# Kernel optimization log

Hardware: AMD Instinct MI355X
Metric: run time of the kernel (lower is better)

## Reference

```python
import jax, jax.numpy as jnp
import numpy as np

DIM = 2048
DIM_HEAD = 128
HEADS = 16
FF_INNER = 4 * DIM  # 8192
ATTN_INNER = DIM_HEAD * HEADS  # 2048
FUSED_DIMS = (ATTN_INNER, DIM_HEAD, DIM_HEAD, FF_INNER * 2)
R = 8
B, N = 2, 2048


def setup_inputs() -> dict:
    key = jax.random.key(0)
    ks = jax.random.split(key, 12)
    s = 0.02
    return {
        "x": jax.random.normal(ks[0], (B, N, DIM), jnp.float32),
        "gamma": jnp.ones((DIM,), jnp.float32),
        "w_fused": jax.random.normal(ks[1], (DIM, sum(FUSED_DIMS)), jnp.float32) * s,
        "w_attn_out": jax.random.normal(ks[2], (ATTN_INNER, DIM), jnp.float32) * s,
        "w_ff_out": jax.random.normal(ks[3], (FF_INNER, DIM), jnp.float32) * s,
        "a_q": jax.random.normal(ks[4], (DIM, R), jnp.float32) * s,
        "b_q": jax.random.normal(ks[5], (R, ATTN_INNER), jnp.float32) * s,
        "a_k": jax.random.normal(ks[6], (DIM, R), jnp.float32) * s,
        "b_k": jax.random.normal(ks[7], (R, DIM_HEAD), jnp.float32) * s,
        "a_v": jax.random.normal(ks[8], (DIM, R), jnp.float32) * s,
        "b_v": jax.random.normal(ks[9], (R, DIM_HEAD), jnp.float32) * s,
        "a_o": jax.random.normal(ks[10], (ATTN_INNER, R), jnp.float32) * s,
        "b_o": jax.random.normal(ks[11], (R, DIM), jnp.float32) * s,
    }


def _rotate_half(t):
    t1, t2 = jnp.split(t, 2, axis=-1)
    return jnp.concatenate((-t2, t1), axis=-1)


def _rope(pos, t):
    return t * jnp.cos(pos) + _rotate_half(t) * jnp.sin(pos)


def reference(x, gamma, w_fused, w_attn_out, w_ff_out,
              a_q, b_q, a_k, b_k, a_v, b_v, a_o, b_o):
    b, n, d = x.shape
    # LayerNorm (beta buffer is zeros)
    mu = jnp.mean(x, -1, keepdims=True)
    var = jnp.var(x, -1, keepdims=True)
    xn = (x - mu) * jax.lax.rsqrt(var + 1e-5) * gamma

    proj = xn @ w_fused
    splits = np.cumsum(FUSED_DIMS)[:-1]
    q, k, v, ff = jnp.split(proj, splits, axis=-1)

    # fused QKV LoRA (scale alpha/r = 1)
    q = q + (xn @ a_q) @ b_q
    k = k + (xn @ a_k) @ b_k
    v = v + (xn @ a_v) @ b_v

    q = q.reshape(b, n, HEADS, DIM_HEAD).transpose(0, 2, 1, 3)  # b h n d
    q = q * (DIM_HEAD ** -0.5)

    # rotary embedding
    inv_freq = 1.0 / (10000.0 ** (jnp.arange(0, DIM_HEAD, 2, dtype=jnp.float32) / DIM_HEAD))
    freqs = jnp.arange(n, dtype=jnp.float32)[:, None] * inv_freq[None, :]  # n, d/2
    pos = jnp.concatenate((freqs, freqs), axis=-1)  # n, d
    q = _rope(pos, q)          # broadcast over b,h
    k = _rope(pos, k)          # b n d (single head, MQA)

    sim = jnp.einsum('bhid,bjd->bhij', q, k)
    causal = jnp.triu(jnp.ones((n, n), dtype=bool), 1)
    sim = jnp.where(causal, -jnp.finfo(sim.dtype).max, sim)
    attn = jax.nn.softmax(sim, axis=-1)
    out = jnp.einsum('bhij,bjd->bhid', attn, v)
    out = out.transpose(0, 2, 1, 3).reshape(b, n, ATTN_INNER)

    attn_out = out @ w_attn_out + (out @ a_o) @ b_o

    x1, gate = jnp.split(ff, 2, axis=-1)
    ff_out = (jax.nn.silu(gate) * x1) @ w_ff_out
    return attn_out + ff_out
```

## Files before the change

kernel.cpp:

```cpp
#include <hip/hip_runtime.h>

typedef unsigned short u16;
typedef __attribute__((ext_vector_type(8))) short s8v;
typedef __attribute__((ext_vector_type(4))) float f32x4;

__device__ __forceinline__ u16 f2bf(float f) {
  unsigned int u = __float_as_uint(f);
  u += ((u >> 16) & 1u) + 0x7FFFu;
  return (u16)(u >> 16);
}
__device__ __forceinline__ float bf2f(u16 h) {
  return __uint_as_float(((unsigned int)h) << 16);
}
__device__ __forceinline__ void gl_lds16(const void* g, void* l) {
  __builtin_amdgcn_global_load_lds(
      (__attribute__((address_space(1))) void*)g,
      (__attribute__((address_space(3))) void*)l, 16, 0, 0);
}
__device__ __forceinline__ f32x4 mfma16(s8v a, s8v b, f32x4 c) {
  return __builtin_amdgcn_mfma_f32_16x16x32_bf16(a, b, c, 0, 0, 0);
}

__global__ void transpose_cvt(const float* __restrict__ in, u16* __restrict__ out,
                              int rows, int cols, int ldo) {
  __shared__ float tile[32][33];
  int c0 = blockIdx.x * 32, r0 = blockIdx.y * 32;
  int tx = threadIdx.x, ty = threadIdx.y;
#pragma unroll
  for (int i = 0; i < 4; i++)
    tile[ty + i * 8][tx] = in[(long)(r0 + ty + i * 8) * cols + c0 + tx];
  __syncthreads();
#pragma unroll
  for (int i = 0; i < 4; i++)
    out[(long)(c0 + ty + i * 8) * ldo + r0 + tx] = f2bf(tile[tx][ty + i * 8]);
}

__global__ void vtrans(const u16* __restrict__ proj, u16* __restrict__ v_t) {
  __shared__ u16 tile[32][33];
  int n0 = blockIdx.x * 32, d0 = blockIdx.y * 32, b = blockIdx.z;
  int tx = threadIdx.x, ty = threadIdx.y;
#pragma unroll
  for (int i = 0; i < 4; i++)
    tile[ty + i * 8][tx] =
        proj[((long)b * 2048 + n0 + ty + i * 8) * 18688 + 2176 + d0 + tx];
  __syncthreads();
#pragma unroll
  for (int i = 0; i < 4; i++)
    v_t[((long)b * 128 + d0 + ty + i * 8) * 2048 + n0 + tx] = tile[tx][ty + i * 8];
}

__global__ void fill_aug_k(u16* __restrict__ wt, int N, int ldo, int naug,
                           const float* __restrict__ bq, const float* __restrict__ bk,
                           const float* __restrict__ bv) {
  long idx = (long)blockIdx.x * 256 + threadIdx.x;
  if (idx >= (long)N * naug) return;
  int n = (int)(idx / naug), j = (int)(idx % naug);
  float v = 0.f;
  if (bq && j < 8 && n < 2048) v = bq[j * 2048 + n];
  else if (bk && j >= 8 && j < 16 && n >= 2048 && n < 2176) v = bk[(j - 8) * 128 + (n - 2048)];
  else if (bv && j >= 16 && j < 24 && n >= 2176 && n < 2304) v = bv[(j - 16) * 128 + (n - 2176)];
  wt[(long)n * ldo + 2048 + j] = f2bf(v);
}

__global__ __launch_bounds__(256) void layernorm_k(const float* __restrict__ x,
                                                   const float* __restrict__ gamma,
                                                   u16* __restrict__ xn) {
  const int row = blockIdx.x, tid = threadIdx.x;
  const float* xr = x + (long)row * 2048 + tid * 8;
  float4 v0 = *(const float4*)xr;
  float4 v1 = *(const float4*)(xr + 4);
  float vals[8] = {v0.x, v0.y, v0.z, v0.w, v1.x, v1.y, v1.z, v1.w};
  float s = 0.f, q = 0.f;
#pragma unroll
  for (int e = 0; e < 8; e++) { s += vals[e]; q += vals[e] * vals[e]; }
#pragma unroll
  for (int off = 32; off > 0; off >>= 1) {
    s += __shfl_down(s, off, 64);
    q += __shfl_down(q, off, 64);
  }
  __shared__ float red[8];
  const int w = tid >> 6, lane = tid & 63;
  if (lane == 0) { red[w] = s; red[4 + w] = q; }
  __syncthreads();
  if (tid == 0) {
    float S = red[0] + red[1] + red[2] + red[3];
    float Q = red[4] + red[5] + red[6] + red[7];
    float mu = S * (1.f / 2048.f);
    float var = Q * (1.f / 2048.f) - mu * mu;
    red[0] = mu; red[1] = rsqrtf(var + 1e-5f);
  }
  __syncthreads();
  float mu = red[0], rs = red[1];
  const float* g = gamma + tid * 8;
  u16 ov[8];
#pragma unroll
  for (int e = 0; e < 8; e++) ov[e] = f2bf((vals[e] - mu) * rs * g[e]);
  *(s8v*)(xn + (long)row * 2112 + tid * 8) = *(const s8v*)ov;
}

__global__ __launch_bounds__(256) void lora_down_x(u16* __restrict__ xn_aug,
                                                   const float* __restrict__ aq,
                                                   const float* __restrict__ ak,
                                                   const float* __restrict__ av) {
  const int row = blockIdx.x, tid = threadIdx.x;
  s8v xv = *(const s8v*)(xn_aug + (long)row * 2112 + tid * 8);
  float acc[3][8];
#pragma unroll
  for (int m = 0; m < 3; m++)
#pragma unroll
    for (int j = 0; j < 8; j++) acc[m][j] = 0.f;
  const float* mats[3] = {aq, ak, av};
#pragma unroll
  for (int e = 0; e < 8; e++) {
    float xe = bf2f((u16)xv[e]);
    int k = tid * 8 + e;
#pragma unroll
    for (int m = 0; m < 3; m++) {
      const float4* ap = (const float4*)(mats[m] + (long)k * 8);
      float4 a0 = ap[0], a1 = ap[1];
      acc[m][0] += xe * a0.x; acc[m][1] += xe * a0.y;
      acc[m][2] += xe * a0.z; acc[m][3] += xe * a0.w;
      acc[m][4] += xe * a1.x; acc[m][5] += xe * a1.y;
      acc[m][6] += xe * a1.z; acc[m][7] += xe * a1.w;
    }
  }
#pragma unroll
  for (int m = 0; m < 3; m++)
#pragma unroll
    for (int j = 0; j < 8; j++)
#pragma unroll
      for (int off = 32; off > 0; off >>= 1)
        acc[m][j] += __shfl_down(acc[m][j], off, 64);
  __shared__ float red[4][24];
  const int w = tid >> 6, lane = tid & 63;
  if (lane == 0)
    for (int m = 0; m < 3; m++)
      for (int j = 0; j < 8; j++) red[w][m * 8 + j] = acc[m][j];
  __syncthreads();
  if (tid < 64) {
    float v = 0.f;
    if (tid < 24) v = red[0][tid] + red[1][tid] + red[2][tid] + red[3][tid];
    xn_aug[(long)row * 2112 + 2048 + tid] = f2bf(v);
  }
}

__global__ __launch_bounds__(256) void lora_down_ctx(u16* __restrict__ ctx_aug,
                                                     const float* __restrict__ ao) {
  const int row = blockIdx.x, tid = threadIdx.x;
  s8v xv = *(const s8v*)(ctx_aug + (long)row * 2080 + tid * 8);
  float acc[8];
#pragma unroll
  for (int j = 0; j < 8; j++) acc[j] = 0.f;
#pragma unroll
  for (int e = 0; e < 8; e++) {
    float xe = bf2f((u16)xv[e]);
    int k = tid * 8 + e;
    const float4* ap = (const float4*)(ao + (long)k * 8);
    float4 a0 = ap[0], a1 = ap[1];
    acc[0] += xe * a0.x; acc[1] += xe * a0.y; acc[2] += xe * a0.z; acc[3] += xe * a0.w;
    acc[4] += xe * a1.x; acc[5] += xe * a1.y; acc[6] += xe * a1.z; acc[7] += xe * a1.w;
  }
#pragma unroll
  for (int j = 0; j < 8; j++)
#pragma unroll
    for (int off = 32; off > 0; off >>= 1)
      acc[j] += __shfl_down(acc[j], off, 64);
  __shared__ float red[4][8];
  const int w = tid >> 6, lane = tid & 63;
  if (lane == 0)
    for (int j = 0; j < 8; j++) red[w][j] = acc[j];
  __syncthreads();
  if (tid < 32) {
    float v = 0.f;
    if (tid < 8) v = red[0][tid] + red[1][tid] + red[2][tid] + red[3][tid];
    ctx_aug[(long)row * 2080 + 2048 + tid] = f2bf(v);
  }
}

__global__ void rope_k(u16* __restrict__ proj) {
  int idx = blockIdx.x * 256 + threadIdx.x;
  int i = idx & 63;
  int u = (idx >> 6) % 17;
  int row = idx / (17 * 64);
  int n = row & 2047;
  float invf = __powf(10000.f, -(float)i * (1.f / 64.f));
  float ang = (float)n * invf;
  float cs = cosf(ang), sn = sinf(ang);
  int cb = (u < 16) ? u * 128 : 2048;
  u16* p = proj + (long)row * 18688 + cb + i;
  float t1 = bf2f(p[0]), t2 = bf2f(p[64]);
  float sc = (u < 16) ? 0.08838834764831845f : 1.f;
  p[0]  = f2bf((t1 * cs - t2 * sn) * sc);
  p[64] = f2bf((t2 * cs + t1 * sn) * sc);
}

__global__ void silu_mul_k(u16* __restrict__ proj) {
  long idx = (long)blockIdx.x * 256 + threadIdx.x;
  int row = (int)(idx >> 10);
  int c8 = (int)(idx & 1023) * 8;
  u16* px = proj + (long)row * 18688 + 2304 + c8;
  const u16* pg = proj + (long)row * 18688 + 10496 + c8;
  s8v xv = *(const s8v*)px;
  s8v gv = *(const s8v*)pg;
  u16 ov[8];
#pragma unroll
  for (int e = 0; e < 8; e++) {
    float x1 = bf2f((u16)xv[e]);
    float g = bf2f((u16)gv[e]);
    ov[e] = f2bf(x1 * g / (1.f + __expf(-g)));
  }
  *(s8v*)px = *(const s8v*)ov;
}

enum { STORE_BF16 = 0, STORE_F32 = 1, ADD_F32 = 2 };
template <int MODE>
__global__ __launch_bounds__(256, 2) void gemm_bt(const u16* __restrict__ A, int lda,
                                                  const u16* __restrict__ Bt, int ldb,
                                                  void* __restrict__ Cv, int ldc, int K,
                                                  int nbx) {
  const int my = blockIdx.x & 31;
  const int mx = blockIdx.y * 8 + (blockIdx.x >> 5);
  if (mx >= nbx) return;
  __shared__ u16 As[128 * 32];
  __shared__ u16 Bs[128 * 32];
  const int tid = threadIdx.x;
  const int w = tid >> 6, lane = tid & 63, quad = lane >> 4, l15 = lane & 15;
  const int wm = (w >> 1) * 64, wn = (w & 1) * 64;
  const long m0 = (long)my * 128;
  const long n0 = (long)mx * 128;

  const int srow = lane >> 2;
  const int scol = (((lane & 3) ^ ((lane >> 3) & 3)) * 8);
  const int cc0 = w * 2, cc1 = cc0 + 1;
  const u16* ga0 = A + (m0 + cc0 * 16 + srow) * lda + scol;
  const u16* ga1 = A + (m0 + cc1 * 16 + srow) * lda + scol;
  const u16* gb0 = Bt + (n0 + cc0 * 16 + srow) * ldb + scol;
  const u16* gb1 = Bt + (n0 + cc1 * 16 + srow) * ldb + scol;
  u16* la0 = As + cc0 * 512;
  u16* la1 = As + cc1 * 512;
  u16* lb0 = Bs + cc0 * 512;
  u16* lb1 = Bs + cc1 * 512;

  const int sseg = (quad ^ ((l15 >> 1) & 3)) * 8;

  f32x4 acc[4][4];
#pragma unroll
  for (int i = 0; i < 4; i++)
#pragma unroll
    for (int j = 0; j < 4; j++) acc[i][j] = {0.f, 0.f, 0.f, 0.f};

  for (int k0 = 0; k0 < K; k0 += 32) {
    gl_lds16(ga0 + k0, la0);
    gl_lds16(ga1 + k0, la1);
    gl_lds16(gb0 + k0, lb0);
    gl_lds16(gb1 + k0, lb1);
    __syncthreads();
    s8v af[4], bf[4];
#pragma unroll
    for (int mi = 0; mi < 4; mi++)
      af[mi] = *(const s8v*)(As + (wm + mi * 16 + l15) * 32 + sseg);
#pragma unroll
    for (int ni = 0; ni < 4; ni++)
      bf[ni] = *(const s8v*)(Bs + (wn + ni * 16 + l15) * 32 + sseg);
#pragma unroll
    for (int mi = 0; mi < 4; mi++)
#pragma unroll
      for (int ni = 0; ni < 4; ni++)
        acc[mi][ni] = mfma16(af[mi], bf[ni], acc[mi][ni]);
    __syncthreads();
  }
#pragma unroll
  for (int mi = 0; mi < 4; mi++)
#pragma unroll
    for (int r = 0; r < 4; r++) {
      long row = m0 + wm + mi * 16 + quad * 4 + r;
#pragma unroll
      for (int ni = 0; ni < 4; ni++) {
        long col = n0 + wn + ni * 16 + l15;
        float v = acc[mi][ni][r];
        if (MODE == STORE_BF16) ((u16*)Cv)[row * ldc + col] = f2bf(v);
        else if (MODE == STORE_F32) ((float*)Cv)[row * ldc + col] = v;
        else ((float*)Cv)[row * ldc + col] += v;
      }
    }
}

__global__ __launch_bounds__(512, 2) void gemm256_bt(const u16* __restrict__ A,
                                                     const u16* __restrict__ Bt,
                                                     u16* __restrict__ C, int K) {
  __shared__ u16 sh[65536];
  const int cpx = gridDim.x >> 3;
  const int swz = (blockIdx.x & 7) * cpx + (blockIdx.x >> 3);
  const int bm = swz & 15;
  const int bn = swz >> 4;
  const int tid = threadIdx.x;
  const int w = tid >> 6, lane = tid & 63;
  const int quad = lane >> 4, l15 = lane & 15;
  const int wm = w >> 2, wn = w & 3;
  const int rseg = (quad ^ ((l15 >> 1) & 3)) * 8;
  const int aoff = (wm * 128 + l15) * 32 + rseg;
  const int boff = (wn * 64 + l15) * 32 + rseg;
  const int srow = lane >> 2;
  const int sseg = ((lane & 3) ^ ((lane >> 3) & 3)) * 8;
  const u16* aSrc = A + (long)(bm * 256 + w * 16 + srow) * 2112 + sseg;
  const u16* bSrc = Bt + (long)(bn * 256 + w * 16 + srow) * 2112 + sseg;
  u16* stW = sh + w * 512;
  const int NT = K >> 6;

  f32x4 acc[8][4];
#pragma unroll
  for (int i = 0; i < 8; i++)
#pragma unroll
    for (int j = 0; j < 4; j++) acc[i][j] = {0.f, 0.f, 0.f, 0.f};

  gl_lds16(aSrc, stW);
  gl_lds16(bSrc, stW + 16384);
  gl_lds16(aSrc + 128L * 2112, stW + 4096);
  gl_lds16(bSrc + 128L * 2112, stW + 16384 + 4096);
  gl_lds16(aSrc + 32, stW + 8192);
  gl_lds16(bSrc + 32, stW + 16384 + 8192);
  gl_lds16(aSrc + 128L * 2112 + 32, stW + 8192 + 4096);
  gl_lds16(bSrc + 128L * 2112 + 32, stW + 16384 + 8192 + 4096);
  asm volatile("s_waitcnt vmcnt(4)" ::: "memory");
  __builtin_amdgcn_s_barrier();

  s8v bf[4];
  int kcol = 64;

#define STAGE_UNIT(CUR, KK, MH)                                               \
  gl_lds16(aSrc + (MH) * (128L * 2112) + kcol + (KK) * 32,                    \
           stW + (((CUR) ^ 1) * 32768) + (KK) * 8192 + (MH) * 4096);          \
  gl_lds16(bSrc + (MH) * (128L * 2112) + kcol + (KK) * 32,                    \
           stW + (((CUR) ^ 1) * 32768) + 16384 + (KK) * 8192 + (MH) * 4096);

#define PHASE(CUR, KK, MH, DOB, STG, VM)                                      \
  {                                                                           \
    const u16* Ab = sh + (CUR) * 32768 + (KK) * 8192 + aoff + (MH) * 2048;    \
    s8v af0 = *(const s8v*)(Ab);                                              \
    s8v af1 = *(const s8v*)(Ab + 512);                                        \
    s8v af2 = *(const s8v*)(Ab + 1024);                                       \
    s8v af3 = *(const s8v*)(Ab + 1536);                                       \
    if (DOB) {                                                                \
      const u16* Bb = sh + (CUR) * 32768 + 16384 + (KK) * 8192 + boff;        \
      bf[0] = *(const s8v*)(Bb);                                              \
      bf[1] = *(const s8v*)(Bb + 512);                                        \
      bf[2] = *(const s8v*)(Bb + 1024);                                       \
      bf[3] = *(const s8v*)(Bb + 1536);                                       \
    }                                                                         \
    if (STG) { STAGE_UNIT(CUR, KK, MH) }                                      \
    __builtin_amdgcn_s_barrier();                                             \
    __builtin_amdgcn_s_setprio(1);                                            \
    _Pragma("unroll") for (int ni = 0; ni < 4; ni++) {                        \
      acc[(MH) * 4 + 0][ni] = mfma16(af0, bf[ni], acc[(MH) * 4 + 0][ni]);     \
      acc[(MH) * 4 + 1][ni] = mfma16(af1, bf[ni], acc[(MH) * 4 + 1][ni]);     \
      acc[(MH) * 4 + 2][ni] = mfma16(af2, bf[ni], acc[(MH) * 4 + 2][ni]);     \
      acc[(MH) * 4 + 3][ni] = mfma16(af3, bf[ni], acc[(MH) * 4 + 3][ni]);     \
    }                                                                         \
    __builtin_amdgcn_s_setprio(0);                                            \
    if ((VM) == 4) asm volatile("s_waitcnt vmcnt(4)" ::: "memory");           \
    if ((VM) == 0) asm volatile("s_waitcnt vmcnt(0)" ::: "memory");           \
    __builtin_amdgcn_s_barrier();                                             \
  }

#define TILE(CUR, STG, VM1, VM3)   \
  PHASE(CUR, 0, 0, 1, STG, -1)     \
  PHASE(CUR, 0, 1, 0, STG, VM1)    \
  PHASE(CUR, 1, 0, 1, STG, -1)     \
  PHASE(CUR, 1, 1, 0, STG, VM3)    \
  kcol += 64;

  for (int t2 = 0; t2 < NT - 1; t2 += 2) {
    TILE(0, 1, 4, 4)
    TILE(1, 1, 4, 4)
  }
  TILE(0, 0, 0, -1)

#undef TILE
#undef PHASE
#undef STAGE_UNIT

  const long m0 = (long)bm * 256 + wm * 128;
  const long n0 = (long)bn * 256 + wn * 64;
#pragma unroll
  for (int mi = 0; mi < 8; mi++)
#pragma unroll
    for (int r = 0; r < 4; r++) {
      long row = m0 + mi * 16 + quad * 4 + r;
#pragma unroll
      for (int ni = 0; ni < 4; ni++) {
        long col = n0 + ni * 16 + l15;
        C[row * 18688 + col] = f2bf(acc[mi][ni][r]);
      }
    }
}

__global__ __launch_bounds__(256) void flash_k(const u16* __restrict__ proj,
                                               const u16* __restrict__ v_t,
                                               u16* __restrict__ ctx) {
  __shared__ u16 Kt[4 * 1024];
  __shared__ u16 Vx[8 * 512];
  __shared__ u16 Pw[4 * 512];
  const int qt = blockIdx.x, h = blockIdx.y, b = blockIdx.z;
  const int tid = threadIdx.x;
  const int w = tid >> 6, lane = tid & 63, quad = lane >> 4, l15 = lane & 15;
  const int qbase = qt * 64 + w * 16;

  s8v qf[4];
  {
    long rowQ = (long)b * 2048 + qbase + l15;
    const u16* qp = proj + rowQ * 18688 + h * 128 + quad * 8;
#pragma unroll
    for (int kk = 0; kk < 4; kk++) qf[kk] = *(const s8v*)(qp + kk * 32);
  }
  f32x4 o[8];
#pragma unroll
  for (int i = 0; i < 8; i++) o[i] = {0.f, 0.f, 0.f, 0.f};
  float m_i[4] = {-1e30f, -1e30f, -1e30f, -1e30f};
  float l_i[4] = {0.f, 0.f, 0.f, 0.f};

  const int srow = lane >> 2;
  const int sseg = ((lane & 3) ^ ((lane >> 3) & 3)) * 8;
  const int rseg = (quad ^ ((l15 >> 1) & 3)) * 8;

  const int nkb = 2 * qt + 2;
  for (int kb = 0; kb < nkb; kb++) {
    const int k0 = kb * 32;
    {
      long rK = (long)b * 2048 + k0;
#pragma unroll
      for (int h2 = 0; h2 < 2; h2++)
        gl_lds16(proj + (rK + h2 * 16 + srow) * 18688 + 2048 + w * 32 + sseg,
                 Kt + w * 1024 + h2 * 512);
#pragma unroll
      for (int h2 = 0; h2 < 2; h2++)
        gl_lds16(v_t + ((long)b * 128 + w * 32 + h2 * 16 + srow) * 2048 + k0 + sseg,
                 Vx + (w * 2 + h2) * 512);
    }
    __syncthreads();
    if (k0 <= qbase + 15) {
      f32x4 s[2];
#pragma unroll
      for (int ni = 0; ni < 2; ni++) {
        f32x4 a = {0.f, 0.f, 0.f, 0.f};
#pragma unroll
        for (int kk = 0; kk < 4; kk++) {
          s8v kf = *(const s8v*)(Kt + kk * 1024 + (ni * 16 + l15) * 32 + rseg);
          a = mfma16(qf[kk], kf, a);
        }
        s[ni] = a;
      }
#pragma unroll
      for (int ni = 0; ni < 2; ni++) {
        int kg = k0 + ni * 16 + l15;
#pragma unroll
        for (int r = 0; r < 4; r++)
          if (kg > qbase + quad * 4 + r) s[ni][r] = -1e30f;
      }
      float al[4];
#pragma unroll
      for (int r = 0; r < 4; r++) {
        float mx = fmaxf(s[0][r], s[1][r]);
#pragma unroll
        for (int off = 8; off > 0; off >>= 1)
          mx = fmaxf(mx, __shfl_xor(mx, off, 16));
        float mn = fmaxf(m_i[r], mx);
        al[r] = __expf(m_i[r] - mn);
        m_i[r] = mn;
      }
#pragma unroll
      for (int ni = 0; ni < 2; ni++)
#pragma unroll
        for (int r = 0; r < 4; r++) s[ni][r] = __expf(s[ni][r] - m_i[r]);
#pragma unroll
      for (int r = 0; r < 4; r++) {
        float rs = s[0][r] + s[1][r];
#pragma unroll
        for (int off = 8; off > 0; off >>= 1)
          rs += __shfl_xor(rs, off, 16);
        l_i[r] = l_i[r] * al[r] + rs;
      }
#pragma unroll
      for (int ni = 0; ni < 2; ni++)
#pragma unroll
        for (int r = 0; r < 4; r++) {
          int p = quad * 4 + r;
          int sg = ni * 2 + (l15 >> 3);
          int sp = sg ^ ((p >> 1) & 3);
          Pw[w * 512 + p * 32 + sp * 8 + (l15 & 7)] = f2bf(s[ni][r]);
        }
      __asm__ volatile("s_waitcnt lgkmcnt(0)" ::: "memory");
#pragma unroll
      for (int nt = 0; nt < 8; nt++)
#pragma unroll
        for (int r = 0; r < 4; r++) o[nt][r] *= al[r];
      s8v pf = *(const s8v*)(Pw + w * 512 + l15 * 32 + rseg);
#pragma unroll
      for (int nt = 0; nt < 8; nt++) {
        s8v vf = *(const s8v*)(Vx + (nt * 16 + l15) * 32 + rseg);
        o[nt] = mfma16(pf, vf, o[nt]);
      }
    }
    __syncthreads();
  }
  float inv[4];
#pragma unroll
  for (int r = 0; r < 4; r++) inv[r] = 1.f / l_i[r];
#pragma unroll
  for (int nt = 0; nt < 8; nt++)
#pragma unroll
    for (int r = 0; r < 4; r++) {
      long row = (long)b * 2048 + qbase + quad * 4 + r;
      ctx[row * 2080 + h * 128 + nt * 16 + l15] = f2bf(o[nt][r] * inv[r]);
    }
}

#define OFF_WF   0L
#define OFF_WO   78938112L
#define OFF_WFF  87457792L
#define OFF_XN   121012224L
#define OFF_PROJ 138313728L
#define WS_NEED  291405824L

extern "C" void kernel_launch(void* const* d_in, const int* in_sizes, int n_in,
                              void* d_out, int out_size, void* d_ws, size_t ws_size,
                              hipStream_t stream) {
  const float* x       = (const float*)d_in[0];
  const float* gamma   = (const float*)d_in[1];
  const float* w_fused = (const float*)d_in[2];
  const float* w_attn  = (const float*)d_in[3];
  const float* w_ff    = (const float*)d_in[4];
  const float* a_q = (const float*)d_in[5];
  const float* b_q = (const float*)d_in[6];
  const float* a_k = (const float*)d_in[7];
  const float* b_k = (const float*)d_in[8];
  const float* a_v = (const float*)d_in[9];
  const float* b_v = (const float*)d_in[10];
  const float* a_o = (const float*)d_in[11];
  const float* b_o = (const float*)d_in[12];
  float* out = (float*)d_out;
  if (ws_size < (size_t)WS_NEED) return;

  char* ws = (char*)d_ws;
  u16* wf_t    = (u16*)(ws + OFF_WF);
  u16* ctx_aug = (u16*)(ws + OFF_WF);
  u16* wo_t    = (u16*)(ws + OFF_WO);
  u16* wff_t   = (u16*)(ws + OFF_WFF);
  u16* xn_aug  = (u16*)(ws + OFF_XN);
  u16* v_t     = (u16*)(ws + OFF_XN);
  u16* proj    = (u16*)(ws + OFF_PROJ);

  dim3 tb(32, 8);
  transpose_cvt<<<dim3(18688 / 32, 2048 / 32), tb, 0, stream>>>(w_fused, wf_t, 2048, 18688, 2112);
  transpose_cvt<<<dim3(2048 / 32, 2048 / 32), tb, 0, stream>>>(w_attn, wo_t, 2048, 2048, 2080);
  transpose_cvt<<<dim3(2048 / 32, 8192 / 32), tb, 0, stream>>>(w_ff, wff_t, 8192, 2048, 8192);
  fill_aug_k<<<(18688 * 64 + 255) / 256, 256, 0, stream>>>(wf_t, 18688, 2112, 64, b_q, b_k, b_v);
  fill_aug_k<<<(2048 * 32 + 255) / 256, 256, 0, stream>>>(wo_t, 2048, 2080, 32, b_o, nullptr, nullptr);

  layernorm_k<<<4096, 256, 0, stream>>>(x, gamma, xn_aug);
  lora_down_x<<<4096, 256, 0, stream>>>(xn_aug, a_q, a_k, a_v);

  gemm256_bt<<<dim3(16 * (18688 / 256)), 512, 0, stream>>>(xn_aug, wf_t, proj, 2112);

  rope_k<<<(4096 * 17 * 64) / 256, 256, 0, stream>>>(proj);
  silu_mul_k<<<(4096 * 1024) / 256, 256, 0, stream>>>(proj);
  vtrans<<<dim3(64, 4, 2), tb, 0, stream>>>(proj, v_t);

  flash_k<<<dim3(32, 16, 2), 256, 0, stream>>>(proj, v_t, ctx_aug);
  lora_down_ctx<<<4096, 256, 0, stream>>>(ctx_aug, a_o);

  gemm_bt<STORE_F32><<<dim3(256, 2), 256, 0, stream>>>(
      ctx_aug, 2080, wo_t, 2080, out, 2048, 2080, 16);
  gemm_bt<ADD_F32><<<dim3(256, 2), 256, 0, stream>>>(
      proj + 2304, 18688, wff_t, 8192, out, 2048, 8192, 16);
}
```

Baseline: 1.383 ms.

## Restructure fused projection GEMM into 4-buffer, 3-deep prefetch pipeline with K=32 stages

The large fused-projection GEMM moves from two LDS buffers of K=64 each to four ring buffers of K=32, keeping three stages in flight (vmcnt(8)) instead of one. The K loop is hard-coded for K=2112 (66 steps of 32), so the runtime K argument is removed. The aim is to hide global-to-LDS latency better behind the MFMA work while total LDS stays the same. In exchange there are more barriers per unit of K, and the kernel now only works for this one K.

```diff
diff --git a/kernel.cpp b/kernel.cpp
--- a/kernel.cpp
+++ b/kernel.cpp
@@ -287,8 +287,8 @@
 
 __global__ __launch_bounds__(512, 2) void gemm256_bt(const u16* __restrict__ A,
                                                      const u16* __restrict__ Bt,
-                                                     u16* __restrict__ C, int K) {
-  __shared__ u16 sh[65536];
+                                                     u16* __restrict__ C) {
+  __shared__ u16 sh[4 * 16384];
   const int cpx = gridDim.x >> 3;
   const int swz = (blockIdx.x & 7) * cpx + (blockIdx.x >> 3);
   const int bm = swz & 15;
@@ -304,8 +304,6 @@
   const int sseg = ((lane & 3) ^ ((lane >> 3) & 3)) * 8;
   const u16* aSrc = A + (long)(bm * 256 + w * 16 + srow) * 2112 + sseg;
   const u16* bSrc = Bt + (long)(bn * 256 + w * 16 + srow) * 2112 + sseg;
-  u16* stW = sh + w * 512;
-  const int NT = K >> 6;
 
   f32x4 acc[8][4];
 #pragma unroll
@@ -313,41 +311,40 @@
 #pragma unroll
     for (int j = 0; j < 4; j++) acc[i][j] = {0.f, 0.f, 0.f, 0.f};
 
-  gl_lds16(aSrc, stW);
-  gl_lds16(bSrc, stW + 16384);
-  gl_lds16(aSrc + 128L * 2112, stW + 4096);
-  gl_lds16(bSrc + 128L * 2112, stW + 16384 + 4096);
-  gl_lds16(aSrc + 32, stW + 8192);
-  gl_lds16(bSrc + 32, stW + 16384 + 8192);
-  gl_lds16(aSrc + 128L * 2112 + 32, stW + 8192 + 4096);
-  gl_lds16(bSrc + 128L * 2112 + 32, stW + 16384 + 8192 + 4096);
-  asm volatile("s_waitcnt vmcnt(4)" ::: "memory");
+#pragma unroll
+  for (int t = 0; t < 3; t++) {
+    gl_lds16(aSrc + t * 32, sh + t * 16384 + w * 512);
+    gl_lds16(bSrc + t * 32, sh + t * 16384 + 8192 + w * 512);
+    gl_lds16(aSrc + 128L * 2112 + t * 32, sh + t * 16384 + 4096 + w * 512);
+    gl_lds16(bSrc + 128L * 2112 + t * 32, sh + t * 16384 + 8192 + 4096 + w * 512);
+  }
+  asm volatile("s_waitcnt vmcnt(8)" ::: "memory");
   __builtin_amdgcn_s_barrier();
 
   s8v bf[4];
-  int kcol = 64;
-
-#define STAGE_UNIT(CUR, KK, MH)                                               \
-  gl_lds16(aSrc + (MH) * (128L * 2112) + kcol + (KK) * 32,                    \
-           stW + (((CUR) ^ 1) * 32768) + (KK) * 8192 + (MH) * 4096);          \
-  gl_lds16(bSrc + (MH) * (128L * 2112) + kcol + (KK) * 32,                    \
-           stW + (((CUR) ^ 1) * 32768) + 16384 + (KK) * 8192 + (MH) * 4096);
-
-#define PHASE(CUR, KK, MH, DOB, STG, VM)                                      \
+  int kcol = 96;
+
+#define STAGE_UNIT(NB, MH)                                                    \
+  gl_lds16(aSrc + (MH) * (128L * 2112) + kcol,                                \
+           sh + (NB) * 16384 + (MH) * 4096 + w * 512);                        \
+  gl_lds16(bSrc + (MH) * (128L * 2112) + kcol,                                \
+           sh + (NB) * 16384 + 8192 + (MH) * 4096 + w * 512);
+
+#define PHASE(CUR, MH, DOB, STG, VM)                                          \
   {                                                                           \
-    const u16* Ab = sh + (CUR) * 32768 + (KK) * 8192 + aoff + (MH) * 2048;    \
+    const u16* Ab = sh + (CUR) * 16384 + aoff + (MH) * 2048;                  \
     s8v af0 = *(const s8v*)(Ab);                                              \
     s8v af1 = *(const s8v*)(Ab + 512);                                        \
     s8v af2 = *(const s8v*)(Ab + 1024);                                       \
     s8v af3 = *(const s8v*)(Ab + 1536);                                       \
     if (DOB) {                                                                \
-      const u16* Bb = sh + (CUR) * 32768 + 16384 + (KK) * 8192 + boff;        \
+      const u16* Bb = sh + (CUR) * 16384 + 8192 + boff;                       \
       bf[0] = *(const s8v*)(Bb);                                              \
       bf[1] = *(const s8v*)(Bb + 512);                                        \
       bf[2] = *(const s8v*)(Bb + 1024);                                       \
       bf[3] = *(const s8v*)(Bb + 1536);                                       \
     }                                                                         \
-    if (STG) { STAGE_UNIT(CUR, KK, MH) }                                      \
+    if (STG) { STAGE_UNIT((((CUR) + 3) & 3), MH) }                            \
     __builtin_amdgcn_s_barrier();                                             \
     __builtin_amdgcn_s_setprio(1);                                            \
     _Pragma("unroll") for (int ni = 0; ni < 4; ni++) {                        \
@@ -357,23 +354,29 @@
       acc[(MH) * 4 + 3][ni] = mfma16(af3, bf[ni], acc[(MH) * 4 + 3][ni]);     \
     }                                                                         \
     __builtin_amdgcn_s_setprio(0);                                            \
+    if ((VM) == 8) asm volatile("s_waitcnt vmcnt(8)" ::: "memory");           \
     if ((VM) == 4) asm volatile("s_waitcnt vmcnt(4)" ::: "memory");           \
     if ((VM) == 0) asm volatile("s_waitcnt vmcnt(0)" ::: "memory");           \
     __builtin_amdgcn_s_barrier();                                             \
   }
 
-#define TILE(CUR, STG, VM1, VM3)   \
-  PHASE(CUR, 0, 0, 1, STG, -1)     \
-  PHASE(CUR, 0, 1, 0, STG, VM1)    \
-  PHASE(CUR, 1, 0, 1, STG, -1)     \
-  PHASE(CUR, 1, 1, 0, STG, VM3)    \
-  kcol += 64;
-
-  for (int t2 = 0; t2 < NT - 1; t2 += 2) {
-    TILE(0, 1, 4, 4)
-    TILE(1, 1, 4, 4)
-  }
-  TILE(0, 0, 0, -1)
+#define TILE(CUR, STG, VM)       \
+  PHASE(CUR, 0, 1, STG, -1)      \
+  PHASE(CUR, 1, 0, STG, VM)      \
+  kcol += 32;
+
+  for (int t4 = 0; t4 < 15; t4++) {
+    TILE(0, 1, 8)
+    TILE(1, 1, 8)
+    TILE(2, 1, 8)
+    TILE(3, 1, 8)
+  }
+  TILE(0, 1, 8)
+  TILE(1, 1, 8)
+  TILE(2, 1, 8)
+  TILE(3, 0, 4)
+  TILE(0, 0, 0)
+  TILE(1, 0, -1)
 
 #undef TILE
 #undef PHASE
@@ -559,7 +562,7 @@
   layernorm_k<<<4096, 256, 0, stream>>>(x, gamma, xn_aug);
   lora_down_x<<<4096, 256, 0, stream>>>(xn_aug, a_q, a_k, a_v);
 
-  gemm256_bt<<<dim3(16 * (18688 / 256)), 512, 0, stream>>>(xn_aug, wf_t, proj, 2112);
+  gemm256_bt<<<dim3(16 * (18688 / 256)), 512, 0, stream>>>(xn_aug, wf_t, proj);
 
   rope_k<<<(4096 * 17 * 64) / 256, 256, 0, stream>>>(proj);
   silu_mul_k<<<(4096 * 1024) / 256, 256, 0, stream>>>(proj);
```

Result: no change. 1.372 ms (-0.8%).
